# Kernel optimization log

Measured on AMD Instinct MI355X. Metric: run time of the kernel, lower is better.

The kernel has to match this reference:

```python
import jax, jax.numpy as jnp
import numpy as np

HIDDEN = 128
HEADS = 8
HEAD_DIM = HIDDEN // HEADS


def setup_inputs() -> dict:
    key = jax.random.key(0)
    ks = jax.random.split(key, 10)
    B, V = 2, 768
    s = 1.0 / np.sqrt(HIDDEN)
    return {
        "x": jax.random.normal(ks[0], (B, V, HIDDEN), dtype=jnp.float32),
        "edge_gate": jax.random.uniform(ks[1], (B, V, V, HIDDEN), dtype=jnp.float32),
        "Wq": jax.random.normal(ks[2], (HIDDEN, HIDDEN), dtype=jnp.float32) * s,
        "bq": jnp.zeros((HIDDEN,), dtype=jnp.float32),
        "Wk": jax.random.normal(ks[3], (HIDDEN, HIDDEN), dtype=jnp.float32) * s,
        "bk": jnp.zeros((HIDDEN,), dtype=jnp.float32),
        "Wv": jax.random.normal(ks[4], (HIDDEN, HIDDEN), dtype=jnp.float32) * s,
        "bv": jnp.zeros((HIDDEN,), dtype=jnp.float32),
        "Wo": jax.random.normal(ks[5], (HIDDEN, HIDDEN), dtype=jnp.float32) * s,
        "bo": jnp.zeros((HIDDEN,), dtype=jnp.float32),
    }


def reference(x, edge_gate, Wq, bq, Wk, bk, Wv, bv, Wo, bo):
    B, V, H = x.shape
    nh, hd = HEADS, HEAD_DIM
    # torch Linear: y = x @ W.T + b
    q = (x @ Wq.T + bq).reshape(B, V, nh, hd).transpose(0, 2, 1, 3)  # (B,nh,V,hd)
    k = (x @ Wk.T + bk).reshape(B, V, nh, hd).transpose(0, 2, 1, 3)
    v = (x @ Wv.T + bv).reshape(B, V, nh, hd).transpose(0, 2, 1, 3)
    scores = jnp.einsum("bhqd,bhkd->bhqk", q, k) / jnp.sqrt(jnp.float32(hd))
    edge_mask = jnp.mean(edge_gate, axis=-1)[:, None]  # (B,1,V,V)
    weights = jax.nn.softmax(scores * edge_mask, axis=-1)
    attended = jnp.einsum("bhqk,bhkd->bhqd", weights, v)
    attended = attended.transpose(0, 2, 1, 3).reshape(B, V, H)
    return attended @ Wo.T + bo
```

## Files before the change

### kernel.cpp

```cpp
#include <hip/hip_runtime.h>
#include <math.h>

#define BB 2
#define VV 768
#define HID 128
#define NH 8
#define HD 16

typedef float f4v __attribute__((ext_vector_type(4)));

__global__ __launch_bounds__(256) void qkv_kernel(
    const float* __restrict__ x,
    const float* __restrict__ Wq, const float* __restrict__ bq,
    const float* __restrict__ Wk, const float* __restrict__ bk,
    const float* __restrict__ Wv, const float* __restrict__ bv,
    float* __restrict__ qh, float* __restrict__ kh, float* __restrict__ vh) {
    __shared__ float xs[2][HID];
    const int half = threadIdx.x >> 7;
    const int c    = threadIdx.x & 127;
    const int row  = blockIdx.x * 2 + half;
    xs[half][c] = x[row * HID + c];
    __syncthreads();
    const float4* xs4 = (const float4*)xs[half];
    const float4* wq4 = (const float4*)(Wq + c * HID);
    const float4* wk4 = (const float4*)(Wk + c * HID);
    const float4* wv4 = (const float4*)(Wv + c * HID);
    float aq = 0.f, ak = 0.f, av = 0.f;
#pragma unroll
    for (int k4 = 0; k4 < HID / 4; ++k4) {
        float4 xv = xs4[k4];
        float4 a = wq4[k4];
        aq += xv.x * a.x + xv.y * a.y + xv.z * a.z + xv.w * a.w;
        float4 bv2 = wk4[k4];
        ak += xv.x * bv2.x + xv.y * bv2.y + xv.z * bv2.z + xv.w * bv2.w;
        float4 cv = wv4[k4];
        av += xv.x * cv.x + xv.y * cv.y + xv.z * cv.z + xv.w * cv.w;
    }
    const int b = row / VV, vi = row - b * VV;
    const int idx = ((b * NH + (c >> 4)) * VV + vi) * HD + (c & 15);
    qh[idx] = aq + bq[c];
    kh[idx] = ak + bk[c];
    vh[idx] = av + bv[c];
}

__global__ __launch_bounds__(256) void fused_edge_attn_out(
    const float* __restrict__ eg,
    const float* __restrict__ qh, const float* __restrict__ kh,
    const float* __restrict__ vh,
    const float* __restrict__ Wo, const float* __restrict__ bo,
    float* __restrict__ out) {
    __shared__ float mask_lds[VV];
    __shared__ float sc_lds[4][VV];
    __shared__ float att_lds[HID];

    const int lane = threadIdx.x & 63;
    const int wid  = threadIdx.x >> 6;
    const int bq   = blockIdx.x;
    const int b    = bq / VV, q = bq - b * VV;

    {
        const float* wbase = eg + (size_t)bq * (VV * HID) + wid * (192 * HID);
#pragma unroll 1
        for (int batch = 0; batch < 12; ++batch) {
            const float* p0 = wbase + batch * 2048 + lane * 4;
            const float* p1 = p0 + 1024;
            f4v v0, v1, v2, v3, v4, v5, v6, v7;
            asm volatile(
                "global_load_dwordx4 %0, %8, off sc0 nt\n\t"
                "global_load_dwordx4 %1, %8, off offset:1024 sc0 nt\n\t"
                "global_load_dwordx4 %2, %8, off offset:2048 sc0 nt\n\t"
                "global_load_dwordx4 %3, %8, off offset:3072 sc0 nt\n\t"
                "global_load_dwordx4 %4, %9, off sc0 nt\n\t"
                "global_load_dwordx4 %5, %9, off offset:1024 sc0 nt\n\t"
                "global_load_dwordx4 %6, %9, off offset:2048 sc0 nt\n\t"
                "global_load_dwordx4 %7, %9, off offset:3072 sc0 nt\n\t"
                "s_waitcnt vmcnt(0)"
                : "=&v"(v0), "=&v"(v1), "=&v"(v2), "=&v"(v3),
                  "=&v"(v4), "=&v"(v5), "=&v"(v6), "=&v"(v7)
                : "v"(p0), "v"(p1));
            const int rbase = wid * 192 + batch * 16 + (lane >> 5);
            float s;
#define REDUCE_ROW(vi, i)                                                  \
            s = ((vi[0] + vi[1]) + (vi[2] + vi[3]));                       \
            s += __shfl_xor(s, 1);  s += __shfl_xor(s, 2);                 \
            s += __shfl_xor(s, 4);  s += __shfl_xor(s, 8);                 \
            s += __shfl_xor(s, 16);                                        \
            if ((lane & 31) == 0)                                          \
                mask_lds[rbase + 2 * (i)] = s * (1.0f / 128.0f);
            REDUCE_ROW(v0, 0) REDUCE_ROW(v1, 1) REDUCE_ROW(v2, 2) REDUCE_ROW(v3, 3)
            REDUCE_ROW(v4, 4) REDUCE_ROW(v5, 5) REDUCE_ROW(v6, 6) REDUCE_ROW(v7, 7)
#undef REDUCE_ROW
        }
    }
    __syncthreads();

#pragma unroll 1
    for (int hh = 0; hh < 2; ++hh) {
        const int h  = wid * 2 + hh;
        const int bh = b * NH + h;
        const float4* qp = (const float4*)(qh + ((size_t)bh * VV + q) * HD);
        const float4 q0 = qp[0], q1 = qp[1], q2 = qp[2], q3 = qp[3];
        const float* kbase = kh + (size_t)bh * VV * HD;
        const float* vbase = vh + (size_t)bh * VV * HD;

        float m = -INFINITY;
#pragma unroll
        for (int t = 0; t < VV / 64; ++t) {
            const int j = lane + 64 * t;
            const float4* kp = (const float4*)(kbase + j * HD);
            float4 k0 = kp[0], k1 = kp[1], k2 = kp[2], k3 = kp[3];
            float dot = q0.x * k0.x + q0.y * k0.y + q0.z * k0.z + q0.w * k0.w
                      + q1.x * k1.x + q1.y * k1.y + q1.z * k1.z + q1.w * k1.w
                      + q2.x * k2.x + q2.y * k2.y + q2.z * k2.z + q2.w * k2.w
                      + q3.x * k3.x + q3.y * k3.y + q3.z * k3.z + q3.w * k3.w;
            float s = dot * 0.25f * mask_lds[j];
            sc_lds[wid][j] = s;
            m = fmaxf(m, s);
        }
#pragma unroll
        for (int off = 1; off < 64; off <<= 1) m = fmaxf(m, __shfl_xor(m, off));

        float sum = 0.f;
        float acc[HD];
#pragma unroll
        for (int d = 0; d < HD; ++d) acc[d] = 0.f;
#pragma unroll
        for (int t = 0; t < VV / 64; ++t) {
            const int j = lane + 64 * t;
            float e = __expf(sc_lds[wid][j] - m);
            sum += e;
            const float4* vp = (const float4*)(vbase + j * HD);
            float4 v0 = vp[0], v1 = vp[1], v2 = vp[2], v3 = vp[3];
            acc[0]  += e * v0.x; acc[1]  += e * v0.y; acc[2]  += e * v0.z; acc[3]  += e * v0.w;
            acc[4]  += e * v1.x; acc[5]  += e * v1.y; acc[6]  += e * v1.z; acc[7]  += e * v1.w;
            acc[8]  += e * v2.x; acc[9]  += e * v2.y; acc[10] += e * v2.z; acc[11] += e * v2.w;
            acc[12] += e * v3.x; acc[13] += e * v3.y; acc[14] += e * v3.z; acc[15] += e * v3.w;
        }
#pragma unroll
        for (int off = 1; off < 64; off <<= 1) sum += __shfl_xor(sum, off);

#pragma unroll
        for (int i = 0; i < 8; ++i) {
            float send = (lane & 1) ? acc[i] : acc[i + 8];
            float r = __shfl_xor(send, 1);
            acc[i] = ((lane & 1) ? acc[i + 8] : acc[i]) + r;
        }
#pragma unroll
        for (int i = 0; i < 4; ++i) {
            float send = (lane & 2) ? acc[i] : acc[i + 4];
            float r = __shfl_xor(send, 2);
            acc[i] = ((lane & 2) ? acc[i + 4] : acc[i]) + r;
        }
#pragma unroll
        for (int i = 0; i < 2; ++i) {
            float send = (lane & 4) ? acc[i] : acc[i + 2];
            float r = __shfl_xor(send, 4);
            acc[i] = ((lane & 4) ? acc[i + 2] : acc[i]) + r;
        }
        {
            float send = (lane & 8) ? acc[0] : acc[1];
            float r = __shfl_xor(send, 8);
            acc[0] = ((lane & 8) ? acc[1] : acc[0]) + r;
        }
        acc[0] += __shfl_xor(acc[0], 16);
        acc[0] += __shfl_xor(acc[0], 32);

        const int d = ((lane & 1) << 3) | ((lane & 2) << 1) | ((lane & 4) >> 1) | ((lane & 8) >> 3);
        if (lane < HD) att_lds[h * HD + d] = acc[0] / sum;
    }
    __syncthreads();

    if (threadIdx.x < HID) {
        const int c = threadIdx.x;
        const float4* a4 = (const float4*)att_lds;
        const float4* w4 = (const float4*)(Wo + c * HID);
        float a = 0.f;
#pragma unroll
        for (int k4 = 0; k4 < HID / 4; ++k4) {
            float4 xv = a4[k4];
            float4 wv = w4[k4];
            a += xv.x * wv.x + xv.y * wv.y + xv.z * wv.z + xv.w * wv.w;
        }
        out[(size_t)bq * HID + c] = a + bo[c];
    }
}

extern "C" void kernel_launch(void* const* d_in, const int* in_sizes, int n_in,
                              void* d_out, int out_size, void* d_ws, size_t ws_size,
                              hipStream_t stream) {
    const float* x  = (const float*)d_in[0];
    const float* eg = (const float*)d_in[1];
    const float* Wq = (const float*)d_in[2];
    const float* bq = (const float*)d_in[3];
    const float* Wk = (const float*)d_in[4];
    const float* bk = (const float*)d_in[5];
    const float* Wv = (const float*)d_in[6];
    const float* bv = (const float*)d_in[7];
    const float* Wo = (const float*)d_in[8];
    const float* bo = (const float*)d_in[9];
    float* out = (float*)d_out;

    float* ws = (float*)d_ws;
    float* qh = ws;
    float* kh = qh + (size_t)BB * VV * HID;
    float* vh = kh + (size_t)BB * VV * HID;

    hipLaunchKernelGGL(qkv_kernel, dim3(BB * VV / 2), dim3(256), 0, stream,
                       x, Wq, bq, Wk, bk, Wv, bv, qh, kh, vh);
    hipLaunchKernelGGL(fused_edge_attn_out, dim3(BB * VV), dim3(256), 0, stream,
                       eg, qh, kh, vh, Wo, bo, out);
}
```

Measured before the change: 265.0 us.

## Reduce edge-gate rows per thread instead of cooperative wave loads with shuffles

Replaces the inline-asm nontemporal dwordx4 loads, where each half-wave reads one 128-float row and reduces it with xor shuffles, with a scheme where each thread sums three whole rows (32 float4 each) serially. This removes the shuffle reductions and the inline asm. In exchange, each wave's loads are now strided by 512 bytes per lane, so accesses are uncoalesced, and the nontemporal cache hints are gone. The edge-gate read dominates the kernel, so the change in memory access pattern is the main risk.

Result: slower. 351.4 us (+32.6%).

```diff
diff --git a/kernel.cpp b/kernel.cpp
--- a/kernel.cpp
+++ b/kernel.cpp
@@ -6,8 +6,6 @@
 #define HID 128
 #define NH 8
 #define HD 16
-
-typedef float f4v __attribute__((ext_vector_type(4)));
 
 __global__ __launch_bounds__(256) void qkv_kernel(
     const float* __restrict__ x,
@@ -59,38 +57,25 @@
     const int b    = bq / VV, q = bq - b * VV;
 
     {
-        const float* wbase = eg + (size_t)bq * (VV * HID) + wid * (192 * HID);
-#pragma unroll 1
-        for (int batch = 0; batch < 12; ++batch) {
-            const float* p0 = wbase + batch * 2048 + lane * 4;
-            const float* p1 = p0 + 1024;
-            f4v v0, v1, v2, v3, v4, v5, v6, v7;
-            asm volatile(
-                "global_load_dwordx4 %0, %8, off sc0 nt\n\t"
-                "global_load_dwordx4 %1, %8, off offset:1024 sc0 nt\n\t"
-                "global_load_dwordx4 %2, %8, off offset:2048 sc0 nt\n\t"
-                "global_load_dwordx4 %3, %8, off offset:3072 sc0 nt\n\t"
-                "global_load_dwordx4 %4, %9, off sc0 nt\n\t"
-                "global_load_dwordx4 %5, %9, off offset:1024 sc0 nt\n\t"
-                "global_load_dwordx4 %6, %9, off offset:2048 sc0 nt\n\t"
-                "global_load_dwordx4 %7, %9, off offset:3072 sc0 nt\n\t"
-                "s_waitcnt vmcnt(0)"
-                : "=&v"(v0), "=&v"(v1), "=&v"(v2), "=&v"(v3),
-                  "=&v"(v4), "=&v"(v5), "=&v"(v6), "=&v"(v7)
-                : "v"(p0), "v"(p1));
-            const int rbase = wid * 192 + batch * 16 + (lane >> 5);
-            float s;
-#define REDUCE_ROW(vi, i)                                                  \
-            s = ((vi[0] + vi[1]) + (vi[2] + vi[3]));                       \
-            s += __shfl_xor(s, 1);  s += __shfl_xor(s, 2);                 \
-            s += __shfl_xor(s, 4);  s += __shfl_xor(s, 8);                 \
-            s += __shfl_xor(s, 16);                                        \
-            if ((lane & 31) == 0)                                          \
-                mask_lds[rbase + 2 * (i)] = s * (1.0f / 128.0f);
-            REDUCE_ROW(v0, 0) REDUCE_ROW(v1, 1) REDUCE_ROW(v2, 2) REDUCE_ROW(v3, 3)
-            REDUCE_ROW(v4, 4) REDUCE_ROW(v5, 5) REDUCE_ROW(v6, 6) REDUCE_ROW(v7, 7)
-#undef REDUCE_ROW
+        const int t = threadIdx.x;
+        const float4* p0 = (const float4*)eg + (size_t)bq * (VV * 32) + (size_t)t * 32;
+        const float4* p1 = p0 + 256 * 32;
+        const float4* p2 = p0 + 512 * 32;
+        float a0x = 0.f, a0y = 0.f, a0z = 0.f, a0w = 0.f;
+        float a1x = 0.f, a1y = 0.f, a1z = 0.f, a1w = 0.f;
+        float a2x = 0.f, a2y = 0.f, a2z = 0.f, a2w = 0.f;
+#pragma unroll
+        for (int k = 0; k < 32; ++k) {
+            float4 v0 = p0[k];
+            a0x += v0.x; a0y += v0.y; a0z += v0.z; a0w += v0.w;
+            float4 v1 = p1[k];
+            a1x += v1.x; a1y += v1.y; a1z += v1.z; a1w += v1.w;
+            float4 v2 = p2[k];
+            a2x += v2.x; a2y += v2.y; a2z += v2.z; a2w += v2.w;
         }
+        mask_lds[t]       = ((a0x + a0y) + (a0z + a0w)) * (1.0f / 128.0f);
+        mask_lds[t + 256] = ((a1x + a1y) + (a1z + a1w)) * (1.0f / 128.0f);
+        mask_lds[t + 512] = ((a2x + a2y) + (a2z + a2w)) * (1.0f / 128.0f);
     }
     __syncthreads();
 
```
